# Optimization experiments

Hardware: AMD Instinct MI355X
Metric: run time of the kernel (lower is better)

The kernel has to match this reference:

```python
import jax, jax.numpy as jnp
import numpy as np

P = 113          # vocab (modulus)
D = 128          # residual_dim
H = 4            # n_heads (hardcoded in Model)
DH = D // H      # head_dim = 32
HID = 4 * D      # mlp hidden = 512
BATCH = 131072
RATE = 0.5       # attention_rate


def setup_inputs() -> dict:
    key = jax.random.key(0)
    ks = jax.random.split(key, 12)
    std = 1.0 / D ** 0.5
    x = jax.random.randint(ks[0], (BATCH, 2), 0, P)
    tok_emb = jax.random.normal(ks[1], (P, D), jnp.float32) / D ** 0.5
    pos_emb = jax.random.normal(ks[2], (2, D), jnp.float32) / D ** 0.5
    W_Q = jax.random.normal(ks[3], (H, D, DH), jnp.float32) * std
    W_K = jax.random.normal(ks[4], (H, D, DH), jnp.float32) * std
    W_V = jax.random.normal(ks[5], (H, D, DH), jnp.float32) * std
    W_O = jax.random.normal(ks[6], (H, DH, D), jnp.float32) * std
    # nn.Linear default init: U(-1/sqrt(fan_in), 1/sqrt(fan_in))
    b1_bound = 1.0 / D ** 0.5
    W1 = jax.random.uniform(ks[7], (D, HID), jnp.float32, -b1_bound, b1_bound)
    b1 = jax.random.uniform(ks[8], (HID,), jnp.float32, -b1_bound, b1_bound)
    b2_bound = 1.0 / HID ** 0.5
    W2 = jax.random.uniform(ks[9], (HID, D), jnp.float32, -b2_bound, b2_bound)
    b2 = jax.random.uniform(ks[10], (D,), jnp.float32, -b2_bound, b2_bound)
    W_U = jax.random.normal(ks[11], (P, D), jnp.float32) / P ** 0.5
    return dict(x=x, tok_emb=tok_emb, pos_emb=pos_emb, W_Q=W_Q, W_K=W_K,
                W_V=W_V, W_O=W_O, W1=W1, b1=b1, W2=W2, b2=b2, W_U=W_U)


def reference(x, tok_emb, pos_emb, W_Q, W_K, W_V, W_O, W1, b1, W2, b2, W_U):
    # embed: [B,2,D]
    resid = tok_emb[x] + pos_emb[None, :, :]
    # attention
    q = jnp.einsum('bpd,hdk->bphk', resid, W_Q)
    k = jnp.einsum('bpd,hdk->bphk', resid, W_K)
    v = jnp.einsum('bpd,hdk->bphk', resid, W_V)
    scores = jnp.einsum('bqhk,bshk->bhqs', q, k) / DH ** 0.5  # [B,H,2,2]
    pattern = jax.nn.softmax(scores, axis=-1)
    pattern = (1.0 - RATE) + RATE * pattern  # uniform blend, no causal mask
    z = jnp.einsum('bshk,bhqs->bqhk', v, pattern)
    attn_out = jnp.einsum('bqhk,hkd->bqd', z, W_O)
    resid = resid + attn_out
    # mlp
    h = jax.nn.relu(resid @ W1 + b1)
    resid = resid + (h @ W2 + b2)
    # unembed: [B,2,P]
    logits = jnp.einsum('vd,bpd->bpv', W_U, resid)
    return logits
```

## Files before the change

kernel.cpp:

```cpp
#include <hip/hip_runtime.h>
#include <hip/hip_bf16.h>
#include <stdint.h>

typedef __hip_bfloat16 bf16;
typedef __attribute__((ext_vector_type(8))) short short8;
typedef __attribute__((ext_vector_type(4))) float float4v;

#define NVOCAB 113
#define NPAIR (113 * 113)
#define DDIM 128
#define HIDDIM 512

#define OFF_TOK 0
#define OFF_POS 14464
#define OFF_WQ  14720
#define OFF_WK  31104
#define OFF_WV  47488
#define OFF_WO  63872
#define OFF_W1  80256
#define OFF_B1  145792
#define OFF_W2  146304
#define OFF_B2  211840
#define OFF_WU  211968
#define WTOTAL  226432

#define BOFF_WOT 0
#define BOFF_W1T 16384
#define BOFF_W2T (16384 + 65536)
#define BOFF_WUP (16384 + 65536 + 65536)
#define BTOTAL   (16384 + 65536 + 65536 + 16384)

__device__ __forceinline__ uint16_t f2b(float f) {
  bf16 h = __float2bfloat16(f);
  return *(uint16_t*)&h;
}

__global__ void detect_kernel(const uint32_t* __restrict__ tok_raw,
                              const uint32_t* __restrict__ x_raw,
                              int* __restrict__ flags) {
  __shared__ int cnt_bf16, cnt_xnz;
  if (threadIdx.x == 0) { cnt_bf16 = 0; cnt_xnz = 0; }
  __syncthreads();
  uint32_t u = tok_raw[threadIdx.x];
  int e = (u >> 7) & 0xff;
  if (e >= 100 && e <= 126) atomicAdd(&cnt_bf16, 1);
  uint32_t xv = x_raw[2 * threadIdx.x + 1];
  if (xv != 0u) atomicAdd(&cnt_xnz, 1);
  __syncthreads();
  if (threadIdx.x == 0) {
    flags[0] = (cnt_bf16 >= 128) ? 1 : 0;
    flags[1] = (cnt_xnz == 0) ? 1 : 0;
  }
}

struct SrcPtrs { const void* p[11]; };

__global__ void convert_kernel(SrcPtrs sp, float* __restrict__ dst,
                               const int* __restrict__ flags) {
  const int idx = blockIdx.x * 256 + threadIdx.x;
  if (idx >= WTOTAL) return;
  const int pref[12] = {OFF_TOK, OFF_POS, OFF_WQ, OFF_WK, OFF_WV, OFF_WO,
                        OFF_W1, OFF_B1, OFF_W2, OFF_B2, OFF_WU, WTOTAL};
  int t = 0;
  while (idx >= pref[t + 1]) ++t;
  const int local = idx - pref[t];
  const void* src = sp.p[t];
  if (flags[0]) {
    dst[idx] = __bfloat162float(((const bf16*)src)[local]);
  } else {
    dst[idx] = ((const float*)src)[local];
  }
}

__global__ void transpose_bf16_kernel(const float* __restrict__ wf,
                                      uint16_t* __restrict__ wb) {
  const int idx = blockIdx.x * 256 + threadIdx.x;
  if (idx >= BTOTAL) return;
  float v;
  if (idx < BOFF_W1T) {
    int l = idx, d = l >> 7, c = l & 127;
    v = wf[OFF_WO + c * 128 + d];
  } else if (idx < BOFF_W2T) {
    int l = idx - BOFF_W1T, n = l >> 7, d = l & 127;
    v = wf[OFF_W1 + d * 512 + n];
  } else if (idx < BOFF_WUP) {
    int l = idx - BOFF_W2T, d = l >> 9, j = l & 511;
    v = wf[OFF_W2 + j * 128 + d];
  } else {
    int l = idx - BOFF_WUP, vv = l >> 7, d = l & 127;
    v = (vv < NVOCAB) ? wf[OFF_WU + vv * 128 + d] : 0.f;
  }
  wb[idx] = f2b(v);
}

__global__ void qkv_kernel(const float* __restrict__ wf,
                           float* __restrict__ resid_pre,
                           float* __restrict__ qt,
                           float* __restrict__ kt,
                           float* __restrict__ vt) {
  const float* tok_emb = wf + OFF_TOK;
  const float* pos_emb = wf + OFF_POS;
  const float* W_Q = wf + OFF_WQ;
  const float* W_K = wf + OFF_WK;
  const float* W_V = wf + OFF_WV;

  const int row = blockIdx.x;
  const int t = row >> 1, p = row & 1;
  const int tid = threadIdx.x;

  __shared__ float r[DDIM];
  float rv = tok_emb[t * DDIM + tid] + pos_emb[p * DDIM + tid];
  r[tid] = rv;
  resid_pre[row * DDIM + tid] = rv;
  __syncthreads();

  const int h = tid >> 5, j = tid & 31;
  const float* wq = W_Q + h * 4096 + j;
  const float* wk = W_K + h * 4096 + j;
  const float* wv = W_V + h * 4096 + j;
  float aq = 0.f, ak = 0.f, av = 0.f;
  #pragma unroll 4
  for (int d = 0; d < DDIM; ++d) {
    float rd = r[d];
    aq += rd * wq[d * 32];
    ak += rd * wk[d * 32];
    av += rd * wv[d * 32];
  }
  qt[row * DDIM + tid] = aq;
  kt[row * DDIM + tid] = ak;
  vt[row * DDIM + tid] = av;
}

__global__ void __launch_bounds__(256) pair_mfma_kernel(
    const float* __restrict__ resid_pre, const float* __restrict__ qt,
    const float* __restrict__ kt, const float* __restrict__ vt,
    const float* __restrict__ wf, const uint16_t* __restrict__ wb,
    float* __restrict__ table) {
  __shared__ uint16_t bufA[32 * 512];
  __shared__ uint16_t bufB[32 * 128];
  __shared__ float    sF[32 * 128];
  __shared__ float    spat[16 * 16];

  const int tid = threadIdx.x;
  const int blk = blockIdx.x;

  {
    const int pl = tid >> 4, s = tid & 15;
    const int pair = blk * 16 + pl;
    if (pair < NPAIR) {
      const int t0 = pair / NVOCAB, t1 = pair - t0 * NVOCAB;
      const int row0 = t0 * 2, row1 = t1 * 2 + 1;
      const int h = s >> 2, qp = (s >> 1) & 1, sp = s & 1;
      const float* qrow = qt + (qp ? row1 : row0) * DDIM + h * 32;
      const float* krow = kt + (sp ? row1 : row0) * DDIM + h * 32;
      float acc = 0.f;
      #pragma unroll
      for (int j = 0; j < 32; ++j) acc += qrow[j] * krow[j];
      spat[pl * 16 + s] = acc * 0.17677669529663687f;
    } else {
      spat[pl * 16 + s] = 0.f;
    }
  }
  __syncthreads();
  {
    const int pl = tid >> 4, s = tid & 15;
    if (s < 8) {
      float s0 = spat[pl * 16 + s * 2], s1 = spat[pl * 16 + s * 2 + 1];
      float m = fmaxf(s0, s1);
      float e0 = __expf(s0 - m), e1 = __expf(s1 - m);
      float inv = 1.f / (e0 + e1);
      spat[pl * 16 + s * 2]     = 0.5f + 0.5f * e0 * inv;
      spat[pl * 16 + s * 2 + 1] = 0.5f + 0.5f * e1 * inv;
    }
  }
  __syncthreads();
  {
    const int pl = tid >> 4, s = tid & 15;
    const int pair = blk * 16 + pl;
    const int qp = s >> 3, c0 = (s & 7) * 16;
    const int m = pl * 2 + qp;
    if (pair < NPAIR) {
      const int t0 = pair / NVOCAB, t1 = pair - t0 * NVOCAB;
      const int row0 = t0 * 2, row1 = t1 * 2 + 1;
      const int rowm = qp ? row1 : row0;
      for (int c = c0; c < c0 + 16; ++c) {
        const int h = c >> 5;
        float p0 = spat[pl * 16 + h * 4 + qp * 2];
        float p1 = spat[pl * 16 + h * 4 + qp * 2 + 1];
        float z = p0 * vt[row0 * DDIM + c] + p1 * vt[row1 * DDIM + c];
        bufA[(m * 16 + ((c >> 3) ^ (m & 15))) * 8 + (c & 7)] = f2b(z);
        sF[m * DDIM + c] = resid_pre[rowm * DDIM + c];
      }
    } else {
      for (int c = c0; c < c0 + 16; ++c) {
        bufA[(m * 16 + ((c >> 3) ^ (m & 15))) * 8 + (c & 7)] = 0;
        sF[m * DDIM + c] = 0.f;
      }
    }
  }
  __syncthreads();

  const int lane = tid & 63, w = tid >> 6;
  const int l15 = lane & 15, quad = lane >> 4;
  const int rowtile = w >> 1, npar = w & 1;
  const int mA = rowtile * 16 + l15;

  {
    short8 af[4];
    #pragma unroll
    for (int ks = 0; ks < 4; ++ks)
      af[ks] = *(const short8*)&bufA[(mA * 16 + ((ks * 4 + quad) ^ (mA & 15))) * 8];
    #pragma unroll
    for (int ni = 0; ni < 4; ++ni) {
      const int n = (npar + ni * 2) * 16 + l15;
      const uint16_t* bp = wb + BOFF_WOT + n * 128 + quad * 8;
      float4v acc = {0.f, 0.f, 0.f, 0.f};
      #pragma unroll
      for (int ks = 0; ks < 4; ++ks) {
        short8 bfv = *(const short8*)(bp + ks * 32);
        acc = __builtin_amdgcn_mfma_f32_16x16x32_bf16(af[ks], bfv, acc, 0, 0, 0);
      }
      #pragma unroll
      for (int r = 0; r < 4; ++r) {
        const int row = rowtile * 16 + quad * 4 + r;
        float v = acc[r] + sF[row * DDIM + n];
        sF[row * DDIM + n] = v;
        bufB[(row * 16 + ((n >> 3) ^ (row & 15))) * 8 + (n & 7)] = f2b(v);
      }
    }
  }
  __syncthreads();

  {
    short8 af[4];
    #pragma unroll
    for (int ks = 0; ks < 4; ++ks)
      af[ks] = *(const short8*)&bufB[(mA * 16 + ((ks * 4 + quad) ^ (mA & 15))) * 8];
    #pragma unroll
    for (int ni = 0; ni < 16; ++ni) {
      const int n = (npar + ni * 2) * 16 + l15;
      const uint16_t* bp = wb + BOFF_W1T + n * 128 + quad * 8;
      float4v acc = {0.f, 0.f, 0.f, 0.f};
      #pragma unroll
      for (int ks = 0; ks < 4; ++ks) {
        short8 bfv = *(const short8*)(bp + ks * 32);
        acc = __builtin_amdgcn_mfma_f32_16x16x32_bf16(af[ks], bfv, acc, 0, 0, 0);
      }
      const float bias = wf[OFF_B1 + n];
      #pragma unroll
      for (int r = 0; r < 4; ++r) {
        const int row = rowtile * 16 + quad * 4 + r;
        float v = fmaxf(acc[r] + bias, 0.f);
        bufA[(row * 64 + ((n >> 3) ^ (row & 15))) * 8 + (n & 7)] = f2b(v);
      }
    }
  }
  __syncthreads();

  {
    short8 af[16];
    #pragma unroll
    for (int ks = 0; ks < 16; ++ks)
      af[ks] = *(const short8*)&bufA[(mA * 64 + ((ks * 4 + quad) ^ (mA & 15))) * 8];
    #pragma unroll
    for (int ni = 0; ni < 4; ++ni) {
      const int n = (npar + ni * 2) * 16 + l15;
      const uint16_t* bp = wb + BOFF_W2T + n * 512 + quad * 8;
      float4v acc = {0.f, 0.f, 0.f, 0.f};
      #pragma unroll
      for (int ks = 0; ks < 16; ++ks) {
        short8 bfv = *(const short8*)(bp + ks * 32);
        acc = __builtin_amdgcn_mfma_f32_16x16x32_bf16(af[ks], bfv, acc, 0, 0, 0);
      }
      const float bias = wf[OFF_B2 + n];
      #pragma unroll
      for (int r = 0; r < 4; ++r) {
        const int row = rowtile * 16 + quad * 4 + r;
        float v = acc[r] + bias + sF[row * DDIM + n];
        bufB[(row * 16 + ((n >> 3) ^ (row & 15))) * 8 + (n & 7)] = f2b(v);
      }
    }
  }
  __syncthreads();

  {
    short8 af[4];
    #pragma unroll
    for (int ks = 0; ks < 4; ++ks)
      af[ks] = *(const short8*)&bufB[(mA * 16 + ((ks * 4 + quad) ^ (mA & 15))) * 8];
    #pragma unroll
    for (int ni = 0; ni < 4; ++ni) {
      const int n = (npar + ni * 2) * 16 + l15;
      const uint16_t* bp = wb + BOFF_WUP + n * 128 + quad * 8;
      float4v acc = {0.f, 0.f, 0.f, 0.f};
      #pragma unroll
      for (int ks = 0; ks < 4; ++ks) {
        short8 bfv = *(const short8*)(bp + ks * 32);
        acc = __builtin_amdgcn_mfma_f32_16x16x32_bf16(af[ks], bfv, acc, 0, 0, 0);
      }
      if (n < NVOCAB) {
        #pragma unroll
        for (int r = 0; r < 4; ++r) {
          const int row = rowtile * 16 + quad * 4 + r;
          const int pair = blk * 16 + (row >> 1);
          const int oq = row & 1;
          if (pair < NPAIR)
            table[pair * 226 + oq * NVOCAB + n] = acc[r];
        }
      }
    }
  }
}

__global__ void gather_kernel(const uint32_t* __restrict__ x_raw,
                              const float2* __restrict__ table_v2,
                              float2* __restrict__ out_v2, int total,
                              const int* __restrict__ flags) {
  __shared__ int is64;
  if (threadIdx.x == 0) is64 = flags[1];
  __syncthreads();
  const int i = blockIdx.x * blockDim.x + threadIdx.x;
  if (i >= total) return;
  const int b = i / NVOCAB;
  const int j = i - b * NVOCAB;
  int t0, t1;
  if (is64) {
    t0 = (int)x_raw[4 * b];
    t1 = (int)x_raw[4 * b + 2];
  } else {
    t0 = (int)x_raw[2 * b];
    t1 = (int)x_raw[2 * b + 1];
  }
  t0 = min(max(t0, 0), NVOCAB - 1);
  t1 = min(max(t1, 0), NVOCAB - 1);
  const int pair = t0 * NVOCAB + t1;
  out_v2[i] = table_v2[pair * NVOCAB + j];
}

extern "C" void kernel_launch(void* const* d_in, const int* in_sizes, int n_in,
                              void* d_out, int out_size, void* d_ws, size_t ws_size,
                              hipStream_t stream) {
  int*      flags     = (int*)d_ws;
  float*    wf        = (float*)((char*)d_ws + 256);
  float*    resid_pre = (float*)((char*)d_ws + 905984);
  float*    qt        = (float*)((char*)d_ws + 1021696);
  float*    kt        = (float*)((char*)d_ws + 1137408);
  float*    vt        = (float*)((char*)d_ws + 1253120);
  float*    table     = (float*)((char*)d_ws + 1368832);
  uint16_t* wb        = (uint16_t*)((char*)d_ws + 12912016);

  const int B = in_sizes[0] / 2;

  detect_kernel<<<1, 256, 0, stream>>>((const uint32_t*)d_in[1],
                                       (const uint32_t*)d_in[0], flags);

  SrcPtrs sp;
  for (int i = 0; i < 11; ++i) sp.p[i] = d_in[i + 1];
  convert_kernel<<<(WTOTAL + 255) / 256, 256, 0, stream>>>(sp, wf, flags);
  transpose_bf16_kernel<<<(BTOTAL + 255) / 256, 256, 0, stream>>>(wf, wb);

  qkv_kernel<<<226, 128, 0, stream>>>(wf, resid_pre, qt, kt, vt);

  const int nblk = (NPAIR + 15) / 16;
  pair_mfma_kernel<<<nblk, 256, 0, stream>>>(resid_pre, qt, kt, vt, wf, wb,
                                             table);

  const int total = B * NVOCAB;
  gather_kernel<<<(total + 255) / 256, 256, 0, stream>>>(
      (const uint32_t*)d_in[0], (const float2*)table, (float2*)d_out,
      total, flags);
}
```

Measured before the change: 279.4 us.

## Shrink pair kernel to 8 pairs per block and bf16-ize QKV weights

The pair MLP kernel now processes 8 token pairs (16 rows) per block instead of 16. Each wave owns one 16-row tile across different output column groups, and it keeps the mid-residual in registers instead of a float shared buffer. The change cuts shared memory and adds a launch-bounds occupancy hint to allow more resident blocks. The QKV projection now reads pre-transposed bf16 weights with vector loads and uses 384 threads, one per output column across Q, K and V. The bf16 QKV weights add rounding error and borrow the table region as scratch, and smaller tiles mean each weight fetch is reused across fewer rows.

Result: faster. 262.8 us (-6.0%).

```diff
diff --git a/kernel.cpp b/kernel.cpp
--- a/kernel.cpp
+++ b/kernel.cpp
@@ -29,10 +29,17 @@
 #define BOFF_W2T (16384 + 65536)
 #define BOFF_WUP (16384 + 65536 + 65536)
 #define BTOTAL   (16384 + 65536 + 65536 + 16384)
+#define QOFF_Q 0
+#define QOFF_K 16384
+#define QOFF_V 32768
+#define QTOTAL 49152
 
 __device__ __forceinline__ uint16_t f2b(float f) {
   bf16 h = __float2bfloat16(f);
   return *(uint16_t*)&h;
+}
+__device__ __forceinline__ float b2f(uint16_t u) {
+  return __uint_as_float(((uint32_t)u) << 16);
 }
 
 __global__ void detect_kernel(const uint32_t* __restrict__ tok_raw,
@@ -73,9 +80,19 @@
 }
 
 __global__ void transpose_bf16_kernel(const float* __restrict__ wf,
-                                      uint16_t* __restrict__ wb) {
+                                      uint16_t* __restrict__ wb,
+                                      uint16_t* __restrict__ qw) {
   const int idx = blockIdx.x * 256 + threadIdx.x;
-  if (idx >= BTOTAL) return;
+  if (idx >= BTOTAL + QTOTAL) return;
+  if (idx >= BTOTAL) {
+    int l = idx - BTOTAL;
+    int which = l >> 14, r = l & 16383;
+    int hj = r >> 7, d = r & 127;
+    int h = hj >> 5, j = hj & 31;
+    int off = (which == 0) ? OFF_WQ : (which == 1) ? OFF_WK : OFF_WV;
+    qw[l] = f2b(wf[off + h * 4096 + d * 32 + j]);
+    return;
+  }
   float v;
   if (idx < BOFF_W1T) {
     int l = idx, d = l >> 7, c = l & 127;
@@ -93,139 +110,136 @@
   wb[idx] = f2b(v);
 }
 
-__global__ void qkv_kernel(const float* __restrict__ wf,
-                           float* __restrict__ resid_pre,
-                           float* __restrict__ qt,
-                           float* __restrict__ kt,
-                           float* __restrict__ vt) {
-  const float* tok_emb = wf + OFF_TOK;
-  const float* pos_emb = wf + OFF_POS;
-  const float* W_Q = wf + OFF_WQ;
-  const float* W_K = wf + OFF_WK;
-  const float* W_V = wf + OFF_WV;
-
+__global__ void __launch_bounds__(384) qkv_kernel(
+    const float* __restrict__ wf, const uint16_t* __restrict__ qw,
+    float* __restrict__ resid_pre, float* __restrict__ qt,
+    float* __restrict__ kt, float* __restrict__ vt) {
   const int row = blockIdx.x;
   const int t = row >> 1, p = row & 1;
   const int tid = threadIdx.x;
 
   __shared__ float r[DDIM];
-  float rv = tok_emb[t * DDIM + tid] + pos_emb[p * DDIM + tid];
-  r[tid] = rv;
-  resid_pre[row * DDIM + tid] = rv;
-  __syncthreads();
-
-  const int h = tid >> 5, j = tid & 31;
-  const float* wq = W_Q + h * 4096 + j;
-  const float* wk = W_K + h * 4096 + j;
-  const float* wv = W_V + h * 4096 + j;
-  float aq = 0.f, ak = 0.f, av = 0.f;
-  #pragma unroll 4
-  for (int d = 0; d < DDIM; ++d) {
-    float rd = r[d];
-    aq += rd * wq[d * 32];
-    ak += rd * wk[d * 32];
-    av += rd * wv[d * 32];
-  }
-  qt[row * DDIM + tid] = aq;
-  kt[row * DDIM + tid] = ak;
-  vt[row * DDIM + tid] = av;
-}
-
-__global__ void __launch_bounds__(256) pair_mfma_kernel(
+  if (tid < DDIM) {
+    float rv = wf[OFF_TOK + t * DDIM + tid] + wf[OFF_POS + p * DDIM + tid];
+    r[tid] = rv;
+    resid_pre[row * DDIM + tid] = rv;
+  }
+  __syncthreads();
+
+  const int which = tid >> 7, j = tid & 127;
+  const short8* wrow = (const short8*)(qw + which * 16384 + j * 128);
+  float a = 0.f;
+  #pragma unroll
+  for (int ch = 0; ch < 16; ++ch) {
+    short8 wv = wrow[ch];
+    #pragma unroll
+    for (int e = 0; e < 8; ++e)
+      a += r[ch * 8 + e] * b2f((uint16_t)wv[e]);
+  }
+  float* outp = (which == 0) ? qt : (which == 1) ? kt : vt;
+  outp[row * DDIM + j] = a;
+}
+
+__global__ void __launch_bounds__(256, 4) pair_mfma_kernel(
     const float* __restrict__ resid_pre, const float* __restrict__ qt,
     const float* __restrict__ kt, const float* __restrict__ vt,
     const float* __restrict__ wf, const uint16_t* __restrict__ wb,
     float* __restrict__ table) {
-  __shared__ uint16_t bufA[32 * 512];
-  __shared__ uint16_t bufB[32 * 128];
-  __shared__ float    sF[32 * 128];
-  __shared__ float    spat[16 * 16];
+  __shared__ uint16_t bufH[16 * 512];
+  __shared__ uint16_t bufZ[16 * 128];
+  __shared__ uint16_t bufS[16 * 128];
+  __shared__ float    spat[8 * 16];
+  __shared__ int      srow[16];
 
   const int tid = threadIdx.x;
   const int blk = blockIdx.x;
 
-  {
+  if (tid < 128) {
     const int pl = tid >> 4, s = tid & 15;
-    const int pair = blk * 16 + pl;
+    const int pair = blk * 8 + pl;
     if (pair < NPAIR) {
       const int t0 = pair / NVOCAB, t1 = pair - t0 * NVOCAB;
       const int row0 = t0 * 2, row1 = t1 * 2 + 1;
       const int h = s >> 2, qp = (s >> 1) & 1, sp = s & 1;
-      const float* qrow = qt + (qp ? row1 : row0) * DDIM + h * 32;
-      const float* krow = kt + (sp ? row1 : row0) * DDIM + h * 32;
+      const float4* qrow = (const float4*)(qt + (qp ? row1 : row0) * DDIM + h * 32);
+      const float4* krow = (const float4*)(kt + (sp ? row1 : row0) * DDIM + h * 32);
       float acc = 0.f;
       #pragma unroll
-      for (int j = 0; j < 32; ++j) acc += qrow[j] * krow[j];
+      for (int j = 0; j < 8; ++j) {
+        float4 qv = qrow[j], kv = krow[j];
+        acc += qv.x * kv.x + qv.y * kv.y + qv.z * kv.z + qv.w * kv.w;
+      }
       spat[pl * 16 + s] = acc * 0.17677669529663687f;
     } else {
       spat[pl * 16 + s] = 0.f;
     }
-  }
-  __syncthreads();
-  {
-    const int pl = tid >> 4, s = tid & 15;
-    if (s < 8) {
-      float s0 = spat[pl * 16 + s * 2], s1 = spat[pl * 16 + s * 2 + 1];
-      float m = fmaxf(s0, s1);
-      float e0 = __expf(s0 - m), e1 = __expf(s1 - m);
-      float inv = 1.f / (e0 + e1);
-      spat[pl * 16 + s * 2]     = 0.5f + 0.5f * e0 * inv;
-      spat[pl * 16 + s * 2 + 1] = 0.5f + 0.5f * e1 * inv;
-    }
-  }
-  __syncthreads();
-  {
-    const int pl = tid >> 4, s = tid & 15;
-    const int pair = blk * 16 + pl;
-    const int qp = s >> 3, c0 = (s & 7) * 16;
-    const int m = pl * 2 + qp;
+  } else if (tid < 144) {
+    const int m = tid - 128;
+    const int pair = blk * 8 + (m >> 1);
+    int rv = 0;
     if (pair < NPAIR) {
       const int t0 = pair / NVOCAB, t1 = pair - t0 * NVOCAB;
-      const int row0 = t0 * 2, row1 = t1 * 2 + 1;
-      const int rowm = qp ? row1 : row0;
-      for (int c = c0; c < c0 + 16; ++c) {
-        const int h = c >> 5;
-        float p0 = spat[pl * 16 + h * 4 + qp * 2];
-        float p1 = spat[pl * 16 + h * 4 + qp * 2 + 1];
-        float z = p0 * vt[row0 * DDIM + c] + p1 * vt[row1 * DDIM + c];
-        bufA[(m * 16 + ((c >> 3) ^ (m & 15))) * 8 + (c & 7)] = f2b(z);
-        sF[m * DDIM + c] = resid_pre[rowm * DDIM + c];
-      }
-    } else {
-      for (int c = c0; c < c0 + 16; ++c) {
-        bufA[(m * 16 + ((c >> 3) ^ (m & 15))) * 8 + (c & 7)] = 0;
-        sF[m * DDIM + c] = 0.f;
-      }
-    }
-  }
-  __syncthreads();
-
-  const int lane = tid & 63, w = tid >> 6;
+      rv = (m & 1) ? t1 * 2 + 1 : t0 * 2;
+    }
+    srow[m] = rv;
+  }
+  __syncthreads();
+  if (tid < 64) {
+    const int pl = tid >> 3, s = tid & 7;
+    const int base = pl * 16 + s * 2;
+    float s0 = spat[base], s1 = spat[base + 1];
+    float m = fmaxf(s0, s1);
+    float e0 = __expf(s0 - m), e1 = __expf(s1 - m);
+    float inv = 1.f / (e0 + e1);
+    spat[base]     = 0.5f + 0.5f * e0 * inv;
+    spat[base + 1] = 0.5f + 0.5f * e1 * inv;
+  }
+  __syncthreads();
+  {
+    const int m = tid >> 4, c0 = (tid & 15) * 8;
+    const int pl = m >> 1, qp = m & 1;
+    const int row0 = srow[pl * 2], row1 = srow[pl * 2 + 1];
+    const int h = c0 >> 5;
+    const float p0 = spat[pl * 16 + h * 4 + qp * 2];
+    const float p1 = spat[pl * 16 + h * 4 + qp * 2 + 1];
+    short8 pk;
+    #pragma unroll
+    for (int e = 0; e < 8; ++e) {
+      const int c = c0 + e;
+      float z = p0 * vt[row0 * DDIM + c] + p1 * vt[row1 * DDIM + c];
+      pk[e] = (short)f2b(z);
+    }
+    *(short8*)&bufZ[(m * 16 + ((c0 >> 3) ^ m)) * 8] = pk;
+  }
+  __syncthreads();
+
+  const int lane = tid & 63;
+  const int npar = tid >> 6;
   const int l15 = lane & 15, quad = lane >> 4;
-  const int rowtile = w >> 1, npar = w & 1;
-  const int mA = rowtile * 16 + l15;
+  const int mA = l15;
+
+  float smid[2][4];
 
   {
     short8 af[4];
     #pragma unroll
     for (int ks = 0; ks < 4; ++ks)
-      af[ks] = *(const short8*)&bufA[(mA * 16 + ((ks * 4 + quad) ^ (mA & 15))) * 8];
-    #pragma unroll
-    for (int ni = 0; ni < 4; ++ni) {
-      const int n = (npar + ni * 2) * 16 + l15;
+      af[ks] = *(const short8*)&bufZ[(mA * 16 + ((ks * 4 + quad) ^ mA)) * 8];
+    #pragma unroll
+    for (int ni = 0; ni < 2; ++ni) {
+      const int n = (npar + ni * 4) * 16 + l15;
       const uint16_t* bp = wb + BOFF_WOT + n * 128 + quad * 8;
       float4v acc = {0.f, 0.f, 0.f, 0.f};
       #pragma unroll
-      for (int ks = 0; ks < 4; ++ks) {
-        short8 bfv = *(const short8*)(bp + ks * 32);
-        acc = __builtin_amdgcn_mfma_f32_16x16x32_bf16(af[ks], bfv, acc, 0, 0, 0);
-      }
+      for (int ks = 0; ks < 4; ++ks)
+        acc = __builtin_amdgcn_mfma_f32_16x16x32_bf16(
+            af[ks], *(const short8*)(bp + ks * 32), acc, 0, 0, 0);
       #pragma unroll
       for (int r = 0; r < 4; ++r) {
-        const int row = rowtile * 16 + quad * 4 + r;
-        float v = acc[r] + sF[row * DDIM + n];
-        sF[row * DDIM + n] = v;
-        bufB[(row * 16 + ((n >> 3) ^ (row & 15))) * 8 + (n & 7)] = f2b(v);
+        const int row = quad * 4 + r;
+        float v = acc[r] + resid_pre[srow[row] * DDIM + n];
+        smid[ni][r] = v;
+        bufS[(row * 16 + ((n >> 3) ^ row)) * 8 + (n & 7)] = f2b(v);
       }
     }
   }
@@ -235,77 +249,73 @@
     short8 af[4];
     #pragma unroll
     for (int ks = 0; ks < 4; ++ks)
-      af[ks] = *(const short8*)&bufB[(mA * 16 + ((ks * 4 + quad) ^ (mA & 15))) * 8];
-    #pragma unroll
-    for (int ni = 0; ni < 16; ++ni) {
-      const int n = (npar + ni * 2) * 16 + l15;
+      af[ks] = *(const short8*)&bufS[(mA * 16 + ((ks * 4 + quad) ^ mA)) * 8];
+    #pragma unroll
+    for (int ni = 0; ni < 8; ++ni) {
+      const int n = (npar + ni * 4) * 16 + l15;
       const uint16_t* bp = wb + BOFF_W1T + n * 128 + quad * 8;
       float4v acc = {0.f, 0.f, 0.f, 0.f};
       #pragma unroll
-      for (int ks = 0; ks < 4; ++ks) {
-        short8 bfv = *(const short8*)(bp + ks * 32);
-        acc = __builtin_amdgcn_mfma_f32_16x16x32_bf16(af[ks], bfv, acc, 0, 0, 0);
-      }
+      for (int ks = 0; ks < 4; ++ks)
+        acc = __builtin_amdgcn_mfma_f32_16x16x32_bf16(
+            af[ks], *(const short8*)(bp + ks * 32), acc, 0, 0, 0);
       const float bias = wf[OFF_B1 + n];
       #pragma unroll
       for (int r = 0; r < 4; ++r) {
-        const int row = rowtile * 16 + quad * 4 + r;
-        float v = fmaxf(acc[r] + bias, 0.f);
-        bufA[(row * 64 + ((n >> 3) ^ (row & 15))) * 8 + (n & 7)] = f2b(v);
-      }
-    }
-  }
-  __syncthreads();
-
-  {
-    short8 af[16];
+        const int row = quad * 4 + r;
+        bufH[(row * 64 + ((n >> 3) ^ row)) * 8 + (n & 7)] =
+            f2b(fmaxf(acc[r] + bias, 0.f));
+      }
+    }
+  }
+  __syncthreads();
+
+  {
+    short8 ah[16];
     #pragma unroll
     for (int ks = 0; ks < 16; ++ks)
-      af[ks] = *(const short8*)&bufA[(mA * 64 + ((ks * 4 + quad) ^ (mA & 15))) * 8];
-    #pragma unroll
-    for (int ni = 0; ni < 4; ++ni) {
-      const int n = (npar + ni * 2) * 16 + l15;
+      ah[ks] = *(const short8*)&bufH[(mA * 64 + ((ks * 4 + quad) ^ mA)) * 8];
+    #pragma unroll
+    for (int ni = 0; ni < 2; ++ni) {
+      const int n = (npar + ni * 4) * 16 + l15;
       const uint16_t* bp = wb + BOFF_W2T + n * 512 + quad * 8;
       float4v acc = {0.f, 0.f, 0.f, 0.f};
       #pragma unroll
-      for (int ks = 0; ks < 16; ++ks) {
-        short8 bfv = *(const short8*)(bp + ks * 32);
-        acc = __builtin_amdgcn_mfma_f32_16x16x32_bf16(af[ks], bfv, acc, 0, 0, 0);
-      }
+      for (int ks = 0; ks < 16; ++ks)
+        acc = __builtin_amdgcn_mfma_f32_16x16x32_bf16(
+            ah[ks], *(const short8*)(bp + ks * 32), acc, 0, 0, 0);
       const float bias = wf[OFF_B2 + n];
       #pragma unroll
       for (int r = 0; r < 4; ++r) {
-        const int row = rowtile * 16 + quad * 4 + r;
-        float v = acc[r] + bias + sF[row * DDIM + n];
-        bufB[(row * 16 + ((n >> 3) ^ (row & 15))) * 8 + (n & 7)] = f2b(v);
-      }
-    }
-  }
-  __syncthreads();
-
-  {
-    short8 af[4];
+        const int row = quad * 4 + r;
+        bufZ[(row * 16 + ((n >> 3) ^ row)) * 8 + (n & 7)] =
+            f2b(acc[r] + bias + smid[ni][r]);
+      }
+    }
+  }
+  __syncthreads();
+
+  {
+    short8 ar[4];
     #pragma unroll
     for (int ks = 0; ks < 4; ++ks)
-      af[ks] = *(const short8*)&bufB[(mA * 16 + ((ks * 4 + quad) ^ (mA & 15))) * 8];
-    #pragma unroll
-    for (int ni = 0; ni < 4; ++ni) {
-      const int n = (npar + ni * 2) * 16 + l15;
+      ar[ks] = *(const short8*)&bufZ[(mA * 16 + ((ks * 4 + quad) ^ mA)) * 8];
+    #pragma unroll
+    for (int ni = 0; ni < 2; ++ni) {
+      const int n = (npar + ni * 4) * 16 + l15;
       const uint16_t* bp = wb + BOFF_WUP + n * 128 + quad * 8;
       float4v acc = {0.f, 0.f, 0.f, 0.f};
       #pragma unroll
-      for (int ks = 0; ks < 4; ++ks) {
-        short8 bfv = *(const short8*)(bp + ks * 32);
-        acc = __builtin_amdgcn_mfma_f32_16x16x32_bf16(af[ks], bfv, acc, 0, 0, 0);
-      }
+      for (int ks = 0; ks < 4; ++ks)
+        acc = __builtin_amdgcn_mfma_f32_16x16x32_bf16(
+            ar[ks], *(const short8*)(bp + ks * 32), acc, 0, 0, 0);
       if (n < NVOCAB) {
         #pragma unroll
         for (int r = 0; r < 4; ++r) {
-          const int row = rowtile * 16 + quad * 4 + r;
-          const int pair = blk * 16 + (row >> 1);
-          const int oq = row & 1;
+          const int row = quad * 4 + r;
+          const int pair = blk * 8 + (row >> 1);
           if (pair < NPAIR)
-            table[pair * 226 + oq * NVOCAB + n] = acc[r];
+            table[pair * 226 + (row & 1) * NVOCAB + n] = acc[r];
         }
       }
     }
@@ -348,6 +358,7 @@
   float*    vt        = (float*)((char*)d_ws + 1253120);
   float*    table     = (float*)((char*)d_ws + 1368832);
   uint16_t* wb        = (uint16_t*)((char*)d_ws + 12912016);
+  uint16_t* qw        = (uint16_t*)table;
 
   const int B = in_sizes[0] / 2;
 
@@ -357,11 +368,12 @@
   SrcPtrs sp;
   for (int i = 0; i < 11; ++i) sp.p[i] = d_in[i + 1];
   convert_kernel<<<(WTOTAL + 255) / 256, 256, 0, stream>>>(sp, wf, flags);
-  transpose_bf16_kernel<<<(BTOTAL + 255) / 256, 256, 0, stream>>>(wf, wb);
-
-  qkv_kernel<<<226, 128, 0, stream>>>(wf, resid_pre, qt, kt, vt);
-
-  const int nblk = (NPAIR + 15) / 16;
+  transpose_bf16_kernel<<<(BTOTAL + QTOTAL + 255) / 256, 256, 0, stream>>>(
+      wf, wb, qw);
+
+  qkv_kernel<<<226, 384, 0, stream>>>(wf, qw, resid_pre, qt, kt, vt);
+
+  const int nblk = (NPAIR + 7) / 8;
   pair_mfma_kernel<<<nblk, 256, 0, stream>>>(resid_pre, qt, kt, vt, wf, wb,
                                              table);
 
```
